# Optimization experiments

Measured on AMD Instinct MI355X. Metric: run time of the kernel, lower is better.

The kernel has to match this reference:

```python
import jax, jax.numpy as jnp
import numpy as np

EPS = 1e-5

def _ln(x, g, b):
    m = jnp.mean(x, axis=-1, keepdims=True)
    v = jnp.mean((x - m) ** 2, axis=-1, keepdims=True)
    return (x - m) * jax.lax.rsqrt(v + EPS) * g + b

def setup_inputs() -> dict:
    key = jax.random.key(0)
    ks = jax.random.split(key, 16)
    B, N, C_IN = 128, 8192, 3
    C1, C2, C3, OUT, IMG = 64, 128, 256, 256, 512
    def lin(k, fan_in, fan_out):
        k1, k2 = jax.random.split(k)
        bound = 1.0 / np.sqrt(fan_in)
        W = jax.random.uniform(k1, (fan_in, fan_out), minval=-bound, maxval=bound, dtype=jnp.float32)
        b = jax.random.uniform(k2, (fan_out,), minval=-bound, maxval=bound, dtype=jnp.float32)
        return W, b
    W1, b1 = lin(ks[0], C_IN, C1)
    W2, b2 = lin(ks[1], C1, C2)
    W3, b3 = lin(ks[2], C2, C3)
    Wp, bp = lin(ks[3], C3, OUT)
    # FiLM generator: weight ~ N(0, 1e-4); bias first half = 1, second half = 0
    Wf = 1e-4 * jax.random.normal(ks[4], (OUT, 2 * IMG), dtype=jnp.float32)
    bf = jnp.concatenate([jnp.ones((IMG,), jnp.float32), jnp.zeros((IMG,), jnp.float32)])
    return {
        "point_cloud": jax.random.normal(ks[5], (B, N, C_IN), dtype=jnp.float32),
        "img_features": jax.random.normal(ks[6], (B, IMG), dtype=jnp.float32),
        "W1": W1, "b1": b1, "g1": jnp.ones((C1,), jnp.float32), "be1": jnp.zeros((C1,), jnp.float32),
        "W2": W2, "b2": b2, "g2": jnp.ones((C2,), jnp.float32), "be2": jnp.zeros((C2,), jnp.float32),
        "W3": W3, "b3": b3, "g3": jnp.ones((C3,), jnp.float32), "be3": jnp.zeros((C3,), jnp.float32),
        "Wp": Wp, "bp": bp, "gp": jnp.ones((OUT,), jnp.float32), "bep": jnp.zeros((OUT,), jnp.float32),
        "Wf": Wf, "bf": bf,
    }

def reference(point_cloud, img_features, W1, b1, g1, be1, W2, b2, g2, be2,
              W3, b3, g3, be3, Wp, bp, gp, bep, Wf, bf):
    # Per-point MLP: Linear -> LayerNorm -> ReLU, three stages
    h = jax.nn.relu(_ln(point_cloud @ W1 + b1, g1, be1))   # (B, N, 64)
    h = jax.nn.relu(_ln(h @ W2 + b2, g2, be2))              # (B, N, 128)
    h = jax.nn.relu(_ln(h @ W3 + b3, g3, be3))              # (B, N, 256)
    pooled = jnp.max(h, axis=1)                              # (B, 256)
    pc_feat = _ln(pooled @ Wp + bp, gp, bep)                 # (B, 256)
    film = pc_feat @ Wf + bf                                 # (B, 1024)
    img_dim = img_features.shape[-1]
    scale, bias = film[:, :img_dim], film[:, img_dim:]
    return scale * img_features + bias                       # (B, 512)
```

## Files before the change

kernel.cpp:

```cpp
#include <hip/hip_runtime.h>

#define EPS 1e-5f

constexpr int Bb  = 128;
constexpr int Np  = 8192;
constexpr int C1  = 64, C2 = 128, C3 = 256;
constexpr int WAVES = 8;
constexpr int P   = 128;
constexpr int CHUNKS = 8;
constexpr int PTS_PER_BLOCK = P * CHUNKS;
constexpr int BLK_PER_BATCH = Np / PTS_PER_BLOCK;

typedef __attribute__((ext_vector_type(8))) short short8v;
typedef __attribute__((ext_vector_type(4))) float f32x4;

__device__ __forceinline__ ushort f2bf(float f) {
  uint x = __float_as_uint(f);
  return (ushort)((x + 0x7fffu + ((x >> 16) & 1u)) >> 16);
}

__device__ __forceinline__ uint cvt_pk_bf16(float lo, float hi) {
  uint r;
  asm("v_cvt_pk_bf16_f32 %0, %1, %2" : "=v"(r) : "v"(lo), "v"(hi));
  return r;
}

__global__ __launch_bounds__(256) void prepW(const float* __restrict__ W2,
                                             const float* __restrict__ W3,
                                             ushort* __restrict__ W2s,
                                             ushort* __restrict__ W3s) {
  const int idx = blockIdx.x * 256 + threadIdx.x;
  if (idx < 8192) {
    const int i  = idx & 7;
    const int l  = (idx >> 3) & 63;
    const int kk = (idx >> 9) & 1;
    const int t  = idx >> 10;
    const int k  = kk * 32 + (l >> 4) * 8 + i;
    const int n  = t * 16 + (l & 15);
    W2s[idx] = f2bf(W2[k * C2 + n]);
  } else {
    const int j  = idx - 8192;
    const int i  = j & 7;
    const int l  = (j >> 3) & 63;
    const int kk = (j >> 9) & 3;
    const int nt = j >> 11;
    const int s  = (l >> 4) * 8 + i;
    const int k  = kk * 32 + (s >> 1) + 16 * (s & 1);
    const int n  = nt * 16 + (l & 15);
    W3s[j] = f2bf(W3[k * C3 + n]);
  }
}

__global__ __launch_bounds__(512) void stageA(
    const float* __restrict__ pc,
    const float* __restrict__ W1, const float* __restrict__ b1,
    const float* __restrict__ g1, const float* __restrict__ be1,
    const ushort* __restrict__ W2s, const float* __restrict__ b2,
    const float* __restrict__ g2, const float* __restrict__ be2,
    const ushort* __restrict__ W3s, const float* __restrict__ b3,
    const float* __restrict__ g3, const float* __restrict__ be3,
    float* __restrict__ pooled)
{
  __shared__ __align__(16) ushort s_w3[32768];
  __shared__ __align__(16) ushort s_w2[8192];
  __shared__ __align__(16) ushort s_h1[WAVES * 1024];
  __shared__ __align__(16) ushort s_h2[WAVES * 2048];
  __shared__ float s_par[1536];

  const int tid  = threadIdx.x;
  const int lane = tid & 63;
  const int w    = tid >> 6;
  const int lrow = lane & 15;
  const int lgrp = lane >> 4;
  const int b    = blockIdx.x >> 3;
  const int base_pt = (blockIdx.x & (BLK_PER_BATCH - 1)) * PTS_PER_BLOCK;

  for (int i = tid; i < 1536; i += 512) {
    float v;
    if      (i <  192) v = W1 [i];
    else if (i <  256) v = b1 [i - 192];
    else if (i <  320) v = g1 [i - 256];
    else if (i <  384) v = be1[i - 320];
    else if (i <  512) v = b2 [i - 384];
    else if (i <  640) v = g2 [i - 512];
    else if (i <  768) v = be2[i - 640];
    else if (i < 1024) v = b3 [i - 768];
    else if (i < 1280) v = g3 [i - 1024];
    else               v = be3[i - 1280];
    s_par[i] = v;
  }
#pragma unroll
  for (int q = 0; q < 2; ++q)
    ((uint4*)s_w2)[q * 512 + tid] = ((const uint4*)W2s)[q * 512 + tid];
#pragma unroll
  for (int q = 0; q < 8; ++q)
    ((uint4*)s_w3)[q * 512 + tid] = ((const uint4*)W3s)[q * 512 + tid];
  __syncthreads();

  char* const h1b = (char*)(s_h1 + w * 1024);
  char* const h2b = (char*)(s_h2 + w * 2048);
  const int sw1 = (lrow & 7) << 4;

  float runmax[16];
#pragma unroll
  for (int t = 0; t < 16; ++t) runmax[t] = 0.f;

  const float* xp0 = pc + (size_t)(b * Np + base_pt + w * 16 + lrow) * 3;
  float x0 = xp0[0], x1 = xp0[1], x2 = xp0[2];

  for (int ch = 0; ch < CHUNKS; ++ch) {
    float y[16];
#pragma unroll
    for (int j = 0; j < 16; ++j) {
      const int c = lgrp * 16 + j;
      y[j] = x0 * s_par[c] + x1 * s_par[64 + c] + x2 * s_par[128 + c] + s_par[192 + c];
    }
    {
      const int chn = (ch + 1 < CHUNKS) ? ch + 1 : ch;
      const float* xpn = pc + (size_t)(b * Np + base_pt + chn * P + w * 16 + lrow) * 3;
      x0 = xpn[0]; x1 = xpn[1]; x2 = xpn[2];
    }
    float s1 = 0.f, q1 = 0.f;
#pragma unroll
    for (int j = 0; j < 16; ++j) { s1 += y[j]; q1 += y[j] * y[j]; }
    s1 += __shfl_xor(s1, 16, 64); q1 += __shfl_xor(q1, 16, 64);
    s1 += __shfl_xor(s1, 32, 64); q1 += __shfl_xor(q1, 32, 64);
    const float m1 = s1 * (1.f / 64.f);
    const float i1 = rsqrtf(q1 * (1.f / 64.f) - m1 * m1 + EPS);
    {
      uint pk[8];
#pragma unroll
      for (int j2 = 0; j2 < 8; ++j2) {
        const int c0 = lgrp * 16 + 2 * j2;
        const float h0 = fmaxf((y[2 * j2]     - m1) * i1 * s_par[256 + c0]     + s_par[320 + c0],     0.f);
        const float h1 = fmaxf((y[2 * j2 + 1] - m1) * i1 * s_par[256 + c0 + 1] + s_par[320 + c0 + 1], 0.f);
        pk[j2] = cvt_pk_bf16(h0, h1);
      }
      const int base = lrow * 128 + lgrp * 32;
      *(uint4*)(h1b + ((base     ) ^ sw1)) = make_uint4(pk[0], pk[1], pk[2], pk[3]);
      *(uint4*)(h1b + ((base + 16) ^ sw1)) = make_uint4(pk[4], pk[5], pk[6], pk[7]);
    }

    short8v a2[2];
#pragma unroll
    for (int kk = 0; kk < 2; ++kk)
      a2[kk] = *(const short8v*)(h1b + ((lrow * 128 + (kk * 64 + lgrp * 16)) ^ sw1));
    {
      f32x4 acc2[8];
      float s2[4] = {0.f,0.f,0.f,0.f}, q2[4] = {0.f,0.f,0.f,0.f};
#pragma unroll
      for (int t = 0; t < 8; ++t) {
        const float bb = s_par[384 + t * 16 + lrow];
        acc2[t] = (f32x4){bb, bb, bb, bb};
#pragma unroll
        for (int kk = 0; kk < 2; ++kk) {
          const short8v w2f = *(const short8v*)((const char*)s_w2 + (((t * 2 + kk) << 6) + lane) * 16);
          acc2[t] = __builtin_amdgcn_mfma_f32_16x16x32_bf16(a2[kk], w2f, acc2[t], 0, 0, 0);
        }
#pragma unroll
        for (int j = 0; j < 4; ++j) {
          const float v = acc2[t][j];
          s2[j] += v; q2[j] += v * v;
        }
      }
#pragma unroll
      for (int m = 1; m < 16; m <<= 1)
#pragma unroll
        for (int j = 0; j < 4; ++j) {
          s2[j] += __shfl_xor(s2[j], m, 64);
          q2[j] += __shfl_xor(q2[j], m, 64);
        }
#pragma unroll
      for (int j = 0; j < 4; ++j) {
        const float m2 = s2[j] * (1.f / 128.f);
        const float i2 = rsqrtf(q2[j] * (1.f / 128.f) - m2 * m2 + EPS);
        const int row = lgrp * 4 + j;
        const int swr = (row & 7) << 4;
        const int rowb = row * 256;
#pragma unroll
        for (int t2 = 0; t2 < 4; ++t2) {
          const int ca = t2 * 32 + lrow, cb = ca + 16;
          const float ha = fmaxf((acc2[2*t2  ][j] - m2) * i2 * s_par[512 + ca] + s_par[640 + ca], 0.f);
          const float hb = fmaxf((acc2[2*t2+1][j] - m2) * i2 * s_par[512 + cb] + s_par[640 + cb], 0.f);
          *(uint*)(h2b + rowb + ((t2 * 64 + lrow * 4) ^ swr)) = cvt_pk_bf16(ha, hb);
        }
      }
    }

    short8v a3[4];
#pragma unroll
    for (int kk = 0; kk < 4; ++kk)
      a3[kk] = *(const short8v*)(h2b + (lrow * 256 + ((kk * 64 + lgrp * 16) ^ sw1)));

    float sj[4] = {0.f,0.f,0.f,0.f}, qj[4] = {0.f,0.f,0.f,0.f};
    uint pA[16];
    {
      f32x4 accA[8];
#pragma unroll
      for (int t = 0; t < 8; ++t) {
        const float bb = s_par[768 + t * 16 + lrow];
        accA[t] = (f32x4){bb, bb, bb, bb};
#pragma unroll
        for (int kk = 0; kk < 4; ++kk) {
          const short8v w3f = *(const short8v*)((const char*)s_w3 + (((t * 4 + kk) << 6) + lane) * 16);
          accA[t] = __builtin_amdgcn_mfma_f32_16x16x32_bf16(a3[kk], w3f, accA[t], 0, 0, 0);
        }
#pragma unroll
        for (int j = 0; j < 4; ++j) { const float v = accA[t][j]; sj[j] += v; qj[j] += v * v; }
      }
#pragma unroll
      for (int t = 0; t < 8; ++t) {
        pA[2*t]   = cvt_pk_bf16(accA[t][0], accA[t][1]);
        pA[2*t+1] = cvt_pk_bf16(accA[t][2], accA[t][3]);
      }
    }
    f32x4 accB[8];
#pragma unroll
    for (int t = 8; t < 16; ++t) {
      const float bb = s_par[768 + t * 16 + lrow];
      accB[t-8] = (f32x4){bb, bb, bb, bb};
#pragma unroll
      for (int kk = 0; kk < 4; ++kk) {
        const short8v w3f = *(const short8v*)((const char*)s_w3 + (((t * 4 + kk) << 6) + lane) * 16);
        accB[t-8] = __builtin_amdgcn_mfma_f32_16x16x32_bf16(a3[kk], w3f, accB[t-8], 0, 0, 0);
      }
#pragma unroll
      for (int j = 0; j < 4; ++j) { const float v = accB[t-8][j]; sj[j] += v; qj[j] += v * v; }
    }
#pragma unroll
    for (int m = 1; m < 16; m <<= 1)
#pragma unroll
      for (int j = 0; j < 4; ++j) {
        sj[j] += __shfl_xor(sj[j], m, 64);
        qj[j] += __shfl_xor(qj[j], m, 64);
      }
    float mean3[4], inv3[4];
#pragma unroll
    for (int j = 0; j < 4; ++j) {
      mean3[j] = sj[j] * (1.f / 256.f);
      inv3[j]  = rsqrtf(qj[j] * (1.f / 256.f) - mean3[j] * mean3[j] + EPS);
    }
#pragma unroll
    for (int t = 8; t < 16; ++t) {
      const int col = t * 16 + lrow;
      const float gg = s_par[1024 + col], ee = s_par[1280 + col];
      float mx = runmax[t];
#pragma unroll
      for (int j = 0; j < 4; ++j)
        mx = fmaxf(mx, fmaxf((accB[t-8][j] - mean3[j]) * inv3[j] * gg + ee, 0.f));
      runmax[t] = mx;
    }
#pragma unroll
    for (int t = 0; t < 8; ++t) {
      const int col = t * 16 + lrow;
      const float gg = s_par[1024 + col], ee = s_par[1280 + col];
      const float v0 = __uint_as_float(pA[2*t]   << 16);
      const float v1 = __uint_as_float(pA[2*t]   & 0xffff0000u);
      const float v2 = __uint_as_float(pA[2*t+1] << 16);
      const float v3 = __uint_as_float(pA[2*t+1] & 0xffff0000u);
      float mx = runmax[t];
      mx = fmaxf(mx, fmaxf((v0 - mean3[0]) * inv3[0] * gg + ee, 0.f));
      mx = fmaxf(mx, fmaxf((v1 - mean3[1]) * inv3[1] * gg + ee, 0.f));
      mx = fmaxf(mx, fmaxf((v2 - mean3[2]) * inv3[2] * gg + ee, 0.f));
      mx = fmaxf(mx, fmaxf((v3 - mean3[3]) * inv3[3] * gg + ee, 0.f));
      runmax[t] = mx;
    }
  }

#pragma unroll
  for (int t = 0; t < 16; ++t) {
    float v = runmax[t];
    v = fmaxf(v, __shfl_xor(v, 16, 64));
    v = fmaxf(v, __shfl_xor(v, 32, 64));
    if (lane < 16)
      atomicMax((int*)&pooled[b * C3 + t * 16 + lane], __float_as_int(v));
  }
}

__global__ __launch_bounds__(256) void stageB(
    const float* __restrict__ pooled,
    const float* __restrict__ img,
    const float* __restrict__ Wp, const float* __restrict__ bp,
    const float* __restrict__ gp, const float* __restrict__ bep,
    const float* __restrict__ Wf, const float* __restrict__ bf,
    float* __restrict__ out)
{
  __shared__ float s_pool[C3];
  __shared__ float s_pc[C3];
  __shared__ float s_red[8];
  __shared__ float s_film[256];

  const int t = threadIdx.x;
  const int b = blockIdx.x >> 2;
  const int qq = blockIdx.x & 3;
  const int lane = t & 63, w = t >> 6;

  s_pool[t] = pooled[b * C3 + t];
  __syncthreads();

  float ya = bp[t], yb = 0.f;
  for (int k = 0; k < C3; k += 2) {
    ya += s_pool[k]     * Wp[k * C3 + t];
    yb += s_pool[k + 1] * Wp[(k + 1) * C3 + t];
  }
  const float y = ya + yb;

  float s = y, q = y * y;
  for (int m = 1; m < 64; m <<= 1) { s += __shfl_xor(s, m, 64); q += __shfl_xor(q, m, 64); }
  if (lane == 0) { s_red[w * 2] = s; s_red[w * 2 + 1] = q; }
  __syncthreads();
  s = s_red[0] + s_red[2] + s_red[4] + s_red[6];
  q = s_red[1] + s_red[3] + s_red[5] + s_red[7];
  const float mean = s * (1.f / 256.f);
  const float var  = q * (1.f / 256.f) - mean * mean;
  const float inv  = rsqrtf(var + EPS);
  s_pc[t] = (y - mean) * inv * gp[t] + bep[t];
  __syncthreads();

  const int cc = qq * 128 + (t & 127) + ((t >> 7) * 512);
  float fa = bf[cc], fb = 0.f;
  for (int k = 0; k < C3; k += 2) {
    fa += s_pc[k]     * Wf[k * 1024 + cc];
    fb += s_pc[k + 1] * Wf[(k + 1) * 1024 + cc];
  }
  s_film[t] = fa + fb;
  __syncthreads();

  if (t < 128) {
    const int col = qq * 128 + t;
    out[b * 512 + col] = s_film[t] * img[b * 512 + col] + s_film[128 + t];
  }
}

extern "C" void kernel_launch(void* const* d_in, const int* in_sizes, int n_in,
                              void* d_out, int out_size, void* d_ws, size_t ws_size,
                              hipStream_t stream) {
  const float* pc  = (const float*)d_in[0];
  const float* img = (const float*)d_in[1];
  const float* W1  = (const float*)d_in[2];
  const float* b1  = (const float*)d_in[3];
  const float* g1  = (const float*)d_in[4];
  const float* be1 = (const float*)d_in[5];
  const float* W2  = (const float*)d_in[6];
  const float* b2  = (const float*)d_in[7];
  const float* g2  = (const float*)d_in[8];
  const float* be2 = (const float*)d_in[9];
  const float* W3  = (const float*)d_in[10];
  const float* b3  = (const float*)d_in[11];
  const float* g3  = (const float*)d_in[12];
  const float* be3 = (const float*)d_in[13];
  const float* Wp  = (const float*)d_in[14];
  const float* bp  = (const float*)d_in[15];
  const float* gp  = (const float*)d_in[16];
  const float* bep = (const float*)d_in[17];
  const float* Wf  = (const float*)d_in[18];
  const float* bf  = (const float*)d_in[19];

  float*  pooled = (float*)d_ws;
  ushort* W2s = (ushort*)((char*)d_ws + Bb * C3 * sizeof(float));
  ushort* W3s = W2s + 8192;

  hipMemsetAsync(pooled, 0, Bb * C3 * sizeof(float), stream);
  prepW<<<160, 256, 0, stream>>>(W2, W3, W2s, W3s);
  stageA<<<Bb * BLK_PER_BATCH, 512, 0, stream>>>(
      pc, W1, b1, g1, be1, W2s, b2, g2, be2, W3s, b3, g3, be3, pooled);
  stageB<<<Bb * 4, 256, 0, stream>>>(pooled, img, Wp, bp, gp, bep, Wf, bf,
                                     (float*)d_out);
}
```

Measured before the change: 360.1 us.

## Compute LayerNorm means via extra MFMA column of summed weights

Appends an extra weight tile holding row sums of W2 and W3, so the per-row mean of each linear output comes from one additional MFMA tile instead of cross-lane shuffle reductions. The layer-1 mean is computed analytically from pre-summed W1 columns. Parameters are interleaved (gamma/beta pairs, W1 rows with bias) to allow vector LDS loads, and normalisation is rewritten as FMAs. The cost is extra MFMAs and LDS, plus the mean now uses bf16-summed weights while the variance uses the actual activations, which can change numerics slightly.

```diff
diff --git a/kernel.cpp b/kernel.cpp
--- a/kernel.cpp
+++ b/kernel.cpp
@@ -18,7 +18,9 @@
   uint x = __float_as_uint(f);
   return (ushort)((x + 0x7fffu + ((x >> 16) & 1u)) >> 16);
 }
-
+__device__ __forceinline__ float bf2f(ushort u) {
+  return __uint_as_float((uint)u << 16);
+}
 __device__ __forceinline__ uint cvt_pk_bf16(float lo, float hi) {
   uint r;
   asm("v_cvt_pk_bf16_f32 %0, %1, %2" : "=v"(r) : "v"(lo), "v"(hi));
@@ -30,24 +32,37 @@
                                              ushort* __restrict__ W2s,
                                              ushort* __restrict__ W3s) {
   const int idx = blockIdx.x * 256 + threadIdx.x;
-  if (idx < 8192) {
+  if (idx >= 44032) return;
+  if (idx < 9216) {
     const int i  = idx & 7;
     const int l  = (idx >> 3) & 63;
     const int kk = (idx >> 9) & 1;
     const int t  = idx >> 10;
     const int k  = kk * 32 + (l >> 4) * 8 + i;
-    const int n  = t * 16 + (l & 15);
-    W2s[idx] = f2bf(W2[k * C2 + n]);
+    if (t < 8) {
+      W2s[idx] = f2bf(W2[k * C2 + t * 16 + (l & 15)]);
+    } else {
+      float s = 0.f;
+      if ((l & 15) == 0)
+        for (int n = 0; n < C2; ++n) s += bf2f(f2bf(W2[k * C2 + n]));
+      W2s[idx] = ((l & 15) == 0) ? f2bf(s) : (ushort)0;
+    }
   } else {
-    const int j  = idx - 8192;
+    const int j  = idx - 9216;
     const int i  = j & 7;
     const int l  = (j >> 3) & 63;
     const int kk = (j >> 9) & 3;
     const int nt = j >> 11;
-    const int s  = (l >> 4) * 8 + i;
-    const int k  = kk * 32 + (s >> 1) + 16 * (s & 1);
-    const int n  = nt * 16 + (l & 15);
-    W3s[j] = f2bf(W3[k * C3 + n]);
+    const int s2 = (l >> 4) * 8 + i;
+    const int k  = kk * 32 + (s2 >> 1) + 16 * (s2 & 1);
+    if (nt < 16) {
+      W3s[j] = f2bf(W3[k * C3 + nt * 16 + (l & 15)]);
+    } else {
+      float s = 0.f;
+      if ((l & 15) == 0)
+        for (int n = 0; n < C3; ++n) s += bf2f(f2bf(W3[k * C3 + n]));
+      W3s[j] = ((l & 15) == 0) ? f2bf(s) : (ushort)0;
+    }
   }
 }
 
@@ -61,8 +76,8 @@
     const float* __restrict__ g3, const float* __restrict__ be3,
     float* __restrict__ pooled)
 {
-  __shared__ __align__(16) ushort s_w3[32768];
-  __shared__ __align__(16) ushort s_w2[8192];
+  __shared__ __align__(16) ushort s_w3[34816];
+  __shared__ __align__(16) ushort s_w2[9216];
   __shared__ __align__(16) ushort s_h1[WAVES * 1024];
   __shared__ __align__(16) ushort s_h2[WAVES * 2048];
   __shared__ float s_par[1536];
@@ -77,25 +92,41 @@
 
   for (int i = tid; i < 1536; i += 512) {
     float v;
-    if      (i <  192) v = W1 [i];
-    else if (i <  256) v = b1 [i - 192];
-    else if (i <  320) v = g1 [i - 256];
-    else if (i <  384) v = be1[i - 320];
-    else if (i <  512) v = b2 [i - 384];
-    else if (i <  640) v = g2 [i - 512];
-    else if (i <  768) v = be2[i - 640];
-    else if (i < 1024) v = b3 [i - 768];
-    else if (i < 1280) v = g3 [i - 1024];
-    else               v = be3[i - 1280];
+    if (i < 256)       { const int q = i & 3, c = i >> 2;
+                         v = (q < 3) ? W1[q * 64 + c] : b1[c]; }
+    else if (i <  384) { const int p = i - 256; v = (p & 1) ? be1[p >> 1] : g1[p >> 1]; }
+    else if (i <  512) { v = b2[i - 384]; }
+    else if (i <  768) { const int p = i - 512; v = (p & 1) ? be2[p >> 1] : g2[p >> 1]; }
+    else if (i < 1024) { v = b3[i - 768]; }
+    else               { const int p = i - 1024; v = (p & 1) ? be3[p >> 1] : g3[p >> 1]; }
     s_par[i] = v;
   }
-#pragma unroll
-  for (int q = 0; q < 2; ++q)
-    ((uint4*)s_w2)[q * 512 + tid] = ((const uint4*)W2s)[q * 512 + tid];
-#pragma unroll
-  for (int q = 0; q < 8; ++q)
-    ((uint4*)s_w3)[q * 512 + tid] = ((const uint4*)W3s)[q * 512 + tid];
+  for (int q = tid; q < 1152; q += 512)
+    ((uint4*)s_w2)[q] = ((const uint4*)W2s)[q];
+  for (int q = tid; q < 4352; q += 512)
+    ((uint4*)s_w3)[q] = ((const uint4*)W3s)[q];
   __syncthreads();
+
+  float w1s0, w1s1, w1s2, b1s;
+  {
+    const float4 wp = *(const float4*)&s_par[4 * lane];
+    w1s0 = wp.x; w1s1 = wp.y; w1s2 = wp.z; b1s = wp.w;
+    for (int m = 1; m < 64; m <<= 1) {
+      w1s0 += __shfl_xor(w1s0, m, 64); w1s1 += __shfl_xor(w1s1, m, 64);
+      w1s2 += __shfl_xor(w1s2, m, 64); b1s  += __shfl_xor(b1s,  m, 64);
+    }
+  }
+  float Sb2, Sb3;
+  {
+    float v2 = s_par[384 + lane] + s_par[384 + 64 + lane];
+    float v3 = 0.f;
+#pragma unroll
+    for (int q = 0; q < 4; ++q) v3 += s_par[768 + lane * 4 + q];
+    for (int m = 1; m < 64; m <<= 1) {
+      v2 += __shfl_xor(v2, m, 64); v3 += __shfl_xor(v3, m, 64);
+    }
+    Sb2 = v2; Sb3 = v3;
+  }
 
   char* const h1b = (char*)(s_h1 + w * 1024);
   char* const h2b = (char*)(s_h2 + w * 2048);
@@ -112,28 +143,32 @@
     float y[16];
 #pragma unroll
     for (int j = 0; j < 16; ++j) {
-      const int c = lgrp * 16 + j;
-      y[j] = x0 * s_par[c] + x1 * s_par[64 + c] + x2 * s_par[128 + c] + s_par[192 + c];
-    }
+      const float4 wp = *(const float4*)&s_par[4 * (lgrp * 16 + j)];
+      y[j] = fmaf(x0, wp.x, fmaf(x1, wp.y, fmaf(x2, wp.z, wp.w)));
+    }
+    const float s1 = fmaf(x0, w1s0, fmaf(x1, w1s1, fmaf(x2, w1s2, b1s)));
     {
       const int chn = (ch + 1 < CHUNKS) ? ch + 1 : ch;
       const float* xpn = pc + (size_t)(b * Np + base_pt + chn * P + w * 16 + lrow) * 3;
       x0 = xpn[0]; x1 = xpn[1]; x2 = xpn[2];
     }
-    float s1 = 0.f, q1 = 0.f;
-#pragma unroll
-    for (int j = 0; j < 16; ++j) { s1 += y[j]; q1 += y[j] * y[j]; }
-    s1 += __shfl_xor(s1, 16, 64); q1 += __shfl_xor(q1, 16, 64);
-    s1 += __shfl_xor(s1, 32, 64); q1 += __shfl_xor(q1, 32, 64);
+    float q1 = 0.f;
+#pragma unroll
+    for (int j = 0; j < 16; ++j) q1 = fmaf(y[j], y[j], q1);
+    q1 += __shfl_xor(q1, 16, 64);
+    q1 += __shfl_xor(q1, 32, 64);
     const float m1 = s1 * (1.f / 64.f);
     const float i1 = rsqrtf(q1 * (1.f / 64.f) - m1 * m1 + EPS);
+    const float M1 = -m1 * i1;
     {
       uint pk[8];
 #pragma unroll
       for (int j2 = 0; j2 < 8; ++j2) {
-        const int c0 = lgrp * 16 + 2 * j2;
-        const float h0 = fmaxf((y[2 * j2]     - m1) * i1 * s_par[256 + c0]     + s_par[320 + c0],     0.f);
-        const float h1 = fmaxf((y[2 * j2 + 1] - m1) * i1 * s_par[256 + c0 + 1] + s_par[320 + c0 + 1], 0.f);
+        const float4 gb = *(const float4*)&s_par[256 + 2 * (lgrp * 16 + 2 * j2)];
+        const float z0 = fmaf(y[2 * j2],     i1, M1);
+        const float z1 = fmaf(y[2 * j2 + 1], i1, M1);
+        const float h0 = fmaxf(fmaf(z0, gb.x, gb.y), 0.f);
+        const float h1 = fmaxf(fmaf(z1, gb.z, gb.w), 0.f);
         pk[j2] = cvt_pk_bf16(h0, h1);
       }
       const int base = lrow * 128 + lgrp * 32;
@@ -146,8 +181,14 @@
     for (int kk = 0; kk < 2; ++kk)
       a2[kk] = *(const short8v*)(h1b + ((lrow * 128 + (kk * 64 + lgrp * 16)) ^ sw1));
     {
+      f32x4 accM = (f32x4){Sb2, Sb2, Sb2, Sb2};
+#pragma unroll
+      for (int kk = 0; kk < 2; ++kk) {
+        const short8v wsf = *(const short8v*)((const char*)s_w2 + (((8 * 2 + kk) << 6) + lane) * 16);
+        accM = __builtin_amdgcn_mfma_f32_16x16x32_bf16(a2[kk], wsf, accM, 0, 0, 0);
+      }
       f32x4 acc2[8];
-      float s2[4] = {0.f,0.f,0.f,0.f}, q2[4] = {0.f,0.f,0.f,0.f};
+      float q2[4] = {0.f, 0.f, 0.f, 0.f};
 #pragma unroll
       for (int t = 0; t < 8; ++t) {
         const float bb = s_par[384 + t * 16 + lrow];
@@ -158,31 +199,32 @@
           acc2[t] = __builtin_amdgcn_mfma_f32_16x16x32_bf16(a2[kk], w2f, acc2[t], 0, 0, 0);
         }
 #pragma unroll
+        for (int j = 0; j < 4; ++j) q2[j] = fmaf(acc2[t][j], acc2[t][j], q2[j]);
+      }
+#pragma unroll
+      for (int m = 1; m < 16; m <<= 1)
+#pragma unroll
+        for (int j = 0; j < 4; ++j) q2[j] += __shfl_xor(q2[j], m, 64);
+      float i2[4], M2[4];
+#pragma unroll
+      for (int j = 0; j < 4; ++j) {
+        const float mu = __shfl(accM[j], lane & 48, 64) * (1.f / 128.f);
+        i2[j] = rsqrtf(q2[j] * (1.f / 128.f) - mu * mu + EPS);
+        M2[j] = -mu * i2[j];
+      }
+#pragma unroll
+      for (int t2 = 0; t2 < 4; ++t2) {
+        const int ca = t2 * 32 + lrow, cb = ca + 16;
+        const float2 gba = *(const float2*)&s_par[512 + 2 * ca];
+        const float2 gbb = *(const float2*)&s_par[512 + 2 * cb];
+#pragma unroll
         for (int j = 0; j < 4; ++j) {
-          const float v = acc2[t][j];
-          s2[j] += v; q2[j] += v * v;
-        }
-      }
-#pragma unroll
-      for (int m = 1; m < 16; m <<= 1)
-#pragma unroll
-        for (int j = 0; j < 4; ++j) {
-          s2[j] += __shfl_xor(s2[j], m, 64);
-          q2[j] += __shfl_xor(q2[j], m, 64);
-        }
-#pragma unroll
-      for (int j = 0; j < 4; ++j) {
-        const float m2 = s2[j] * (1.f / 128.f);
-        const float i2 = rsqrtf(q2[j] * (1.f / 128.f) - m2 * m2 + EPS);
-        const int row = lgrp * 4 + j;
-        const int swr = (row & 7) << 4;
-        const int rowb = row * 256;
-#pragma unroll
-        for (int t2 = 0; t2 < 4; ++t2) {
-          const int ca = t2 * 32 + lrow, cb = ca + 16;
-          const float ha = fmaxf((acc2[2*t2  ][j] - m2) * i2 * s_par[512 + ca] + s_par[640 + ca], 0.f);
-          const float hb = fmaxf((acc2[2*t2+1][j] - m2) * i2 * s_par[512 + cb] + s_par[640 + cb], 0.f);
-          *(uint*)(h2b + rowb + ((t2 * 64 + lrow * 4) ^ swr)) = cvt_pk_bf16(ha, hb);
+          const float za = fmaf(acc2[2 * t2    ][j], i2[j], M2[j]);
+          const float zb = fmaf(acc2[2 * t2 + 1][j], i2[j], M2[j]);
+          const float ha = fmaxf(fmaf(za, gba.x, gba.y), 0.f);
+          const float hb = fmaxf(fmaf(zb, gbb.x, gbb.y), 0.f);
+          const int row = lgrp * 4 + j;
+          *(uint*)(h2b + row * 256 + ((t2 * 64 + lrow * 4) ^ ((row & 7) << 4))) = cvt_pk_bf16(ha, hb);
         }
       }
     }
@@ -192,7 +234,14 @@
     for (int kk = 0; kk < 4; ++kk)
       a3[kk] = *(const short8v*)(h2b + (lrow * 256 + ((kk * 64 + lgrp * 16) ^ sw1)));
 
-    float sj[4] = {0.f,0.f,0.f,0.f}, qj[4] = {0.f,0.f,0.f,0.f};
+    f32x4 accM3 = (f32x4){Sb3, Sb3, Sb3, Sb3};
+#pragma unroll
+    for (int kk = 0; kk < 4; ++kk) {
+      const short8v wsf = *(const short8v*)((const char*)s_w3 + ((((16 * 4) + kk) << 6) + lane) * 16);
+      accM3 = __builtin_amdgcn_mfma_f32_16x16x32_bf16(a3[kk], wsf, accM3, 0, 0, 0);
+    }
+
+    float qj[4] = {0.f, 0.f, 0.f, 0.f};
     uint pA[16];
     {
       f32x4 accA[8];
@@ -206,63 +255,61 @@
           accA[t] = __builtin_amdgcn_mfma_f32_16x16x32_bf16(a3[kk], w3f, accA[t], 0, 0, 0);
         }
 #pragma unroll
-        for (int j = 0; j < 4; ++j) { const float v = accA[t][j]; sj[j] += v; qj[j] += v * v; }
+        for (int j = 0; j < 4; ++j) qj[j] = fmaf(accA[t][j], accA[t][j], qj[j]);
       }
 #pragma unroll
       for (int t = 0; t < 8; ++t) {
-        pA[2*t]   = cvt_pk_bf16(accA[t][0], accA[t][1]);
-        pA[2*t+1] = cvt_pk_bf16(accA[t][2], accA[t][3]);
+        pA[2 * t]     = cvt_pk_bf16(accA[t][0], accA[t][1]);
+        pA[2 * t + 1] = cvt_pk_bf16(accA[t][2], accA[t][3]);
       }
     }
     f32x4 accB[8];
 #pragma unroll
     for (int t = 8; t < 16; ++t) {
       const float bb = s_par[768 + t * 16 + lrow];
-      accB[t-8] = (f32x4){bb, bb, bb, bb};
+      accB[t - 8] = (f32x4){bb, bb, bb, bb};
 #pragma unroll
       for (int kk = 0; kk < 4; ++kk) {
         const short8v w3f = *(const short8v*)((const char*)s_w3 + (((t * 4 + kk) << 6) + lane) * 16);
-        accB[t-8] = __builtin_amdgcn_mfma_f32_16x16x32_bf16(a3[kk], w3f, accB[t-8], 0, 0, 0);
-      }
-#pragma unroll
-      for (int j = 0; j < 4; ++j) { const float v = accB[t-8][j]; sj[j] += v; qj[j] += v * v; }
+        accB[t - 8] = __builtin_amdgcn_mfma_f32_16x16x32_bf16(a3[kk], w3f, accB[t - 8], 0, 0, 0);
+      }
+#pragma unroll
+      for (int j = 0; j < 4; ++j) qj[j] = fmaf(accB[t - 8][j], accB[t - 8][j], qj[j]);
     }
 #pragma unroll
     for (int m = 1; m < 16; m <<= 1)
 #pragma unroll
+      for (int j = 0; j < 4; ++j) qj[j] += __shfl_xor(qj[j], m, 64);
+    float i3[4], M3[4];
+#pragma unroll
+    for (int j = 0; j < 4; ++j) {
+      const float mu = __shfl(accM3[j], lane & 48, 64) * (1.f / 256.f);
+      i3[j] = rsqrtf(qj[j] * (1.f / 256.f) - mu * mu + EPS);
+      M3[j] = -mu * i3[j];
+    }
+#pragma unroll
+    for (int t = 8; t < 16; ++t) {
+      const float2 gb = *(const float2*)&s_par[1024 + 2 * (t * 16 + lrow)];
+      float mx = runmax[t];
+#pragma unroll
       for (int j = 0; j < 4; ++j) {
-        sj[j] += __shfl_xor(sj[j], m, 64);
-        qj[j] += __shfl_xor(qj[j], m, 64);
-      }
-    float mean3[4], inv3[4];
-#pragma unroll
-    for (int j = 0; j < 4; ++j) {
-      mean3[j] = sj[j] * (1.f / 256.f);
-      inv3[j]  = rsqrtf(qj[j] * (1.f / 256.f) - mean3[j] * mean3[j] + EPS);
-    }
-#pragma unroll
-    for (int t = 8; t < 16; ++t) {
-      const int col = t * 16 + lrow;
-      const float gg = s_par[1024 + col], ee = s_par[1280 + col];
+        const float z = fmaf(accB[t - 8][j], i3[j], M3[j]);
+        mx = fmaxf(mx, fmaxf(fmaf(z, gb.x, gb.y), 0.f));
+      }
+      runmax[t] = mx;
+    }
+#pragma unroll
+    for (int t = 0; t < 8; ++t) {
+      const float2 gb = *(const float2*)&s_par[1024 + 2 * (t * 16 + lrow)];
+      const float v0 = __uint_as_float(pA[2 * t]     << 16);
+      const float v1 = __uint_as_float(pA[2 * t]     & 0xffff0000u);
+      const float v2 = __uint_as_float(pA[2 * t + 1] << 16);
+      const float v3 = __uint_as_float(pA[2 * t + 1] & 0xffff0000u);
       float mx = runmax[t];
-#pragma unroll
-      for (int j = 0; j < 4; ++j)
-        mx = fmaxf(mx, fmaxf((accB[t-8][j] - mean3[j]) * inv3[j] * gg + ee, 0.f));
-      runmax[t] = mx;
-    }
-#pragma unroll
-    for (int t = 0; t < 8; ++t) {
-      const int col = t * 16 + lrow;
-      const float gg = s_par[1024 + col], ee = s_par[1280 + col];
-      const float v0 = __uint_as_float(pA[2*t]   << 16);
-      const float v1 = __uint_as_float(pA[2*t]   & 0xffff0000u);
-      const float v2 = __uint_as_float(pA[2*t+1] << 16);
-      const float v3 = __uint_as_float(pA[2*t+1] & 0xffff0000u);
-      float mx = runmax[t];
-      mx = fmaxf(mx, fmaxf((v0 - mean3[0]) * inv3[0] * gg + ee, 0.f));
-      mx = fmaxf(mx, fmaxf((v1 - mean3[1]) * inv3[1] * gg + ee, 0.f));
-      mx = fmaxf(mx, fmaxf((v2 - mean3[2]) * inv3[2] * gg + ee, 0.f));
-      mx = fmaxf(mx, fmaxf((v3 - mean3[3]) * inv3[3] * gg + ee, 0.f));
+      mx = fmaxf(mx, fmaxf(fmaf(fmaf(v0, i3[0], M3[0]), gb.x, gb.y), 0.f));
+      mx = fmaxf(mx, fmaxf(fmaf(fmaf(v1, i3[1], M3[1]), gb.x, gb.y), 0.f));
+      mx = fmaxf(mx, fmaxf(fmaf(fmaf(v2, i3[2], M3[2]), gb.x, gb.y), 0.f));
+      mx = fmaxf(mx, fmaxf(fmaf(fmaf(v3, i3[3], M3[3]), gb.x, gb.y), 0.f));
       runmax[t] = mx;
     }
   }
@@ -357,11 +404,11 @@
   const float* bf  = (const float*)d_in[19];
 
   float*  pooled = (float*)d_ws;
-  ushort* W2s = (ushort*)((char*)d_ws + Bb * C3 * sizeof(float));
-  ushort* W3s = W2s + 8192;
+  ushort* W2s = (ushort*)((char*)d_ws + 131072);
+  ushort* W3s = (ushort*)((char*)d_ws + 131072 + 18432);
 
   hipMemsetAsync(pooled, 0, Bb * C3 * sizeof(float), stream);
-  prepW<<<160, 256, 0, stream>>>(W2, W3, W2s, W3s);
+  prepW<<<172, 256, 0, stream>>>(W2, W3, W2s, W3s);
   stageA<<<Bb * BLK_PER_BATCH, 512, 0, stream>>>(
       pc, W1, b1, g1, be1, W2s, b2, g2, be2, W3s, b3, g3, be3, pooled);
   stageB<<<Bb * 4, 256, 0, stream>>>(pooled, img, Wp, bp, gp, bep, Wf, bf,
```

Result: faster. 313.1 us (-13.0%).
